# Kernel tuning notes

Measured on AMD Instinct MI355X. Metric: run time of the kernel, lower is better.

Reference implementation:

```python
import jax, jax.numpy as jnp
import numpy as np

LOGIT_SCALE = 1.0
REDUCTION = "mean"

N, H, V = 4096, 512, 50257


def setup_inputs() -> dict:
    key = jax.random.key(0)
    k1, k2, k3, k4 = jax.random.split(key, 4)
    x = jax.random.normal(k1, (N, H), dtype=jnp.float32)
    targets = jax.random.normal(k2, (N, V), dtype=jnp.float32)
    weight = jax.random.normal(k3, (V, H), dtype=jnp.float32) * 0.02
    bias = jax.random.normal(k4, (V,), dtype=jnp.float32) * 0.02
    return {"x": x, "targets": targets, "weight": weight, "bias": bias}


def reference(x, targets, weight, bias):
    # logits = x @ W^T + b  -> [N, V]
    logits = jnp.einsum("nh,vh->nv", x, weight) + bias
    scaled = logits * LOGIT_SCALE
    # logsumexp over vocab for both predicted and target logits (fp32)
    lse_logits = jax.nn.logsumexp(scaled, axis=-1)                      # [N]
    lse_targets = jax.nn.logsumexp(targets, axis=-1)                    # [N]
    # original: .nan_to_num(nan=inf) -> rows with nan targets contribute 0
    lse_targets = jnp.where(jnp.isnan(lse_targets), jnp.inf, lse_targets)
    p_target = jnp.exp(targets - lse_targets[:, None])                  # softmax(targets)
    log_p_pred = scaled - lse_logits[:, None]                           # log_softmax(scaled logits)
    per_row_loss = -jnp.sum(p_target * log_p_pred, axis=-1)             # [N]
    loss = per_row_loss.sum()
    if REDUCTION == "mean":
        loss = loss / N
    return loss
```

## Files before the change

kernel.cpp:

```cpp
#include <hip/hip_runtime.h>
#include <hip/hip_bf16.h>

#define N_ROWS 4096
#define H_DIM  512
#define V_DIM  50257
#define BM 128
#define BN 128
#define BK 64
#define NSTEP (H_DIM / BK)
#define VT_TOTAL 393
#define V_PAD (VT_TOTAL * BN)
#define NCHUNK 131
#define LOG2E 1.4426950408889634f
#define BUF0 0
#define BUF1 32768
#define LBASE 32768

#define VMCNT8() asm volatile("s_waitcnt vmcnt(8)" ::: "memory")
#define VMCNT0() asm volatile("s_waitcnt vmcnt(0)" ::: "memory")
#define LGKM0()  asm volatile("s_waitcnt lgkmcnt(0)" ::: "memory")
#define BARRIER() __builtin_amdgcn_s_barrier()

typedef __attribute__((ext_vector_type(8))) short short8;
typedef __attribute__((ext_vector_type(4))) float f32x4;

static __device__ __forceinline__ unsigned short f2bf(float f) {
  unsigned u = __float_as_uint(f);
  u = (u + 0x7fffu + ((u >> 16) & 1u)) >> 16;
  return (unsigned short)u;
}

static __device__ __forceinline__ void gload_lds16(const void* g, void* l) {
  __builtin_amdgcn_global_load_lds(
      (const __attribute__((address_space(1))) void*)g,
      (__attribute__((address_space(3))) void*)l, 16, 0, 0);
}

__global__ void convert_kernel(const float* __restrict__ X,
                               const float* __restrict__ W,
                               __hip_bfloat16* __restrict__ Xb,
                               __hip_bfloat16* __restrict__ Wb) {
  const long wtot8 = (long)V_PAD * H_DIM / 8;
  const long xtot8 = (long)N_ROWS * H_DIM / 8;
  long i = (long)blockIdx.x * blockDim.x + threadIdx.x;
  unsigned short o[8];
  if (i < wtot8) {
    long base = i * 8;
    long row = base >> 9;
    if (row < V_DIM) {
      const float4* s = (const float4*)(W + base);
      float4 a = s[0], b = s[1];
      o[0]=f2bf(a.x); o[1]=f2bf(a.y); o[2]=f2bf(a.z); o[3]=f2bf(a.w);
      o[4]=f2bf(b.x); o[5]=f2bf(b.y); o[6]=f2bf(b.z); o[7]=f2bf(b.w);
    } else {
      #pragma unroll
      for (int k = 0; k < 8; ++k) o[k] = 0;
    }
    *(short8*)(Wb + base) = *(const short8*)o;
  } else if (i < wtot8 + xtot8) {
    long base = (i - wtot8) * 8;
    const float4* s = (const float4*)(X + base);
    float4 a = s[0], b = s[1];
    o[0]=f2bf(a.x); o[1]=f2bf(a.y); o[2]=f2bf(a.z); o[3]=f2bf(a.w);
    o[4]=f2bf(b.x); o[5]=f2bf(b.y); o[6]=f2bf(b.z); o[7]=f2bf(b.w);
    *(short8*)(Xb + base) = *(const short8*)o;
  }
}

template <bool GUARD>
static __device__ __forceinline__ void chunk_stats(
    const float (&Lraw)[16], const f32x4 (&T)[4], int gcol0,
    float& mlr, float& slr, float& mtr, float& str, float& ddr) {
  float Lv[16], Tv[16];
  #pragma unroll
  for (int k = 0; k < 16; ++k) {
    const bool ok = !GUARD || (gcol0 + k < V_DIM);
    Lv[k] = ok ? Lraw[k] : -1e30f;
    Tv[k] = ok ? T[k >> 2][k & 3] : -1e30f;
  }
  float g = Lv[0];
  #pragma unroll
  for (int k = 1; k < 16; ++k) g = fmaxf(g, Lv[k]);
  if (g > mlr + 12.f) { slr *= exp2f((mlr - g) * LOG2E); mlr = g; }
  float bl = mlr * LOG2E;
  float ss = 0.f;
  #pragma unroll
  for (int k = 0; k < 16; ++k) ss += exp2f(__builtin_fmaf(Lv[k], LOG2E, -bl));
  slr += ss;
  float gt = Tv[0];
  #pragma unroll
  for (int k = 1; k < 16; ++k) gt = fmaxf(gt, Tv[k]);
  if (gt > mtr + 12.f) {
    float sc = exp2f((mtr - gt) * LOG2E);
    str *= sc; ddr *= sc; mtr = gt;
  }
  float bt = mtr * LOG2E;
  float s2 = 0.f, d2 = 0.f;
  #pragma unroll
  for (int k = 0; k < 16; ++k) {
    float e = exp2f(__builtin_fmaf(Tv[k], LOG2E, -bt));
    s2 += e;
    d2 = __builtin_fmaf(e, Lv[k], d2);
  }
  str += s2; ddr += d2;
}

template <bool GUARD>
static __device__ __forceinline__ void stream_tile(
    const float* __restrict__ targets, const char* __restrict__ Lrow,
    long growVD, int vbase, int cb0, int rsw, long tlim,
    float& mlr, float& slr, float& mtr, float& str, float& ddr) {
  f32x4 T0[4], T1[4];
  auto LOADT = [&](f32x4 (&D)[4], int i) {
    #pragma unroll
    for (int c = 0; c < 4; ++c) {
      long off = growVD + vbase + cb0 + i * 16 + c * 4;
      if (GUARD) off = off > tlim ? tlim : off;
      D[c] = *(const f32x4*)(targets + off);
    }
  };
  auto DOCHUNK = [&](const f32x4 (&T)[4], int i) {
    const int ob = (cb0 << 1) + (i << 5);
    short8 l0 = *(const short8*)(Lrow + ((ob) ^ rsw));
    short8 l1 = *(const short8*)(Lrow + ((ob + 16) ^ rsw));
    float Lraw[16];
    #pragma unroll
    for (int e = 0; e < 8; ++e) {
      Lraw[e]     = __uint_as_float(((unsigned)(unsigned short)l0[e]) << 16);
      Lraw[e + 8] = __uint_as_float(((unsigned)(unsigned short)l1[e]) << 16);
    }
    chunk_stats<GUARD>(Lraw, T, vbase + cb0 + i * 16, mlr, slr, mtr, str, ddr);
  };
  LOADT(T0, 0); LOADT(T1, 1);
  DOCHUNK(T0, 0);
  LOADT(T0, 2);
  DOCHUNK(T1, 1);
  LOADT(T1, 3);
  DOCHUNK(T0, 2);
  DOCHUNK(T1, 3);
}

__global__ __launch_bounds__(256, 2)
void fused_kernel(const __hip_bfloat16* __restrict__ Xb,
                  const __hip_bfloat16* __restrict__ Wb,
                  const float* __restrict__ bias,
                  const float* __restrict__ targets,
                  float* __restrict__ partials) {
  __shared__ __align__(16) char smem[65536];

  const int tid  = threadIdx.x;
  const int lane = tid & 63;
  const int wid  = tid >> 6;
  const int wm   = wid >> 1;
  const int wn   = wid & 1;
  const int q    = lane >> 4;
  const int c15  = lane & 15;
  const int brow = blockIdx.x;
  const int chunk = blockIdx.y;

  float mlr = -1e30f, slr = 0.f, mtr = -1e30f, str = 0.f, ddr = 0.f;

  const int srow8 = tid >> 3;
  const int soff  = ((tid & 7) * 8) ^ ((srow8 & 7) * 8);
  const __hip_bfloat16* asrc = Xb + (long)(brow * BM + srow8) * H_DIM + soff;

  const int rm      = (c15 & 7) << 4;
  const int arow_b  = (wm * 64 + c15) * 128;
  const int brow_b  = (wn * 64 + c15) * 128;

  auto stage = [&](int bufb, const __hip_bfloat16* a_s,
                   const __hip_bfloat16* b_s, int kk) {
    #pragma unroll
    for (int i = 0; i < 4; ++i)
      gload_lds16(a_s + (long)i * 32 * H_DIM + kk,
                  smem + bufb + i * 4096 + tid * 16);
    #pragma unroll
    for (int i = 0; i < 4; ++i)
      gload_lds16(b_s + (long)i * 32 * H_DIM + kk,
                  smem + bufb + 16384 + i * 4096 + tid * 16);
  };

  const int srow  = tid >> 1;
  const int shalf = tid & 1;
  const int cb0   = shalf * 64;
  const long grow   = (long)(brow * BM + srow);
  const long growVD = grow * V_DIM;
  const long tlim   = (long)N_ROWS * V_DIM - 4;
  const char* Lrow  = smem + LBASE + srow * 256;
  const int rsw     = (srow & 7) << 4;

  const __hip_bfloat16* bsrc = Wb + (long)(chunk * BN + srow8) * H_DIM + soff;
  stage(BUF0, asrc, bsrc, 0);

  #pragma unroll 1
  for (int vt = chunk; vt < VT_TOTAL; vt += NCHUNK) {
    const int vbase = vt * BN;
    const int v0 = vbase + wn * 64 + q * 4;
    const bool last = (vt + NCHUNK >= VT_TOTAL);
    const __hip_bfloat16* bsrc_next =
        Wb + (long)((vt + NCHUNK) * BN + srow8) * H_DIM + soff;

    f32x4 acc[4][4];
    #pragma unroll
    for (int a = 0; a < 4; ++a)
      #pragma unroll
      for (int b = 0; b < 4; ++b)
        acc[a][b] = (f32x4){0.f, 0.f, 0.f, 0.f};

    #pragma unroll
    for (int ks = 0; ks < NSTEP; ++ks) {
      const int cb = (ks & 1) ? BUF1 : BUF0;
      const int nb = cb ^ 32768;
      if (ks < NSTEP - 1)
        stage(nb, asrc, bsrc, (ks + 1) * BK);
      else if (!last)
        stage(nb, asrc, bsrc_next, 0);

      if (ks == NSTEP - 1 && last) { VMCNT0(); } else { VMCNT8(); }
      BARRIER();

      #pragma unroll
      for (int s = 0; s < 2; ++s) {
        short8 xf[4], wf[4];
        #pragma unroll
        for (int a = 0; a < 4; ++a)
          xf[a] = *(const short8*)(smem + cb + arow_b + a * 2048 +
                                   ((s * 64 + q * 16) ^ rm));
        #pragma unroll
        for (int b = 0; b < 4; ++b)
          wf[b] = *(const short8*)(smem + cb + 16384 + brow_b + b * 2048 +
                                   ((s * 64 + q * 16) ^ rm));
        __builtin_amdgcn_s_setprio(1);
        #pragma unroll
        for (int a = 0; a < 4; ++a)
          #pragma unroll
          for (int b = 0; b < 4; ++b)
            acc[a][b] = __builtin_amdgcn_mfma_f32_16x16x32_bf16(
                wf[b], xf[a], acc[a][b], 0, 0, 0);
        __builtin_amdgcn_s_setprio(0);
      }
      LGKM0();
      BARRIER();
    }
    bsrc = bsrc_next;

    f32x4 bp[4];
    #pragma unroll
    for (int b = 0; b < 4; ++b) {
      int bo = v0 + b * 16;
      bo = bo > (V_DIM - 4) ? (V_DIM - 4) : bo;
      bp[b] = *(const f32x4*)(bias + bo);
    }
    #pragma unroll
    for (int a = 0; a < 4; ++a) {
      const int row = wm * 64 + a * 16 + c15;
      char* rb = smem + LBASE + row * 256;
      #pragma unroll
      for (int b = 0; b < 4; ++b) {
        uint2 w;
        w.x = (unsigned)f2bf(acc[a][b][0] + bp[b][0]) |
              ((unsigned)f2bf(acc[a][b][1] + bp[b][1]) << 16);
        w.y = (unsigned)f2bf(acc[a][b][2] + bp[b][2]) |
              ((unsigned)f2bf(acc[a][b][3] + bp[b][3]) << 16);
        const int o = wn * 128 + b * 32 + q * 8;
        *(uint2*)(rb + (o ^ rm)) = w;
      }
    }
    LGKM0();
    BARRIER();

    if (vt == VT_TOTAL - 1)
      stream_tile<true >(targets, Lrow, growVD, vbase, cb0, rsw, tlim,
                         mlr, slr, mtr, str, ddr);
    else
      stream_tile<false>(targets, Lrow, growVD, vbase, cb0, rsw, tlim,
                         mlr, slr, mtr, str, ddr);
    LGKM0();
    BARRIER();
  }

  {
    float ml2 = __shfl_xor(mlr, 1);
    float sl2 = __shfl_xor(slr, 1);
    float mt2 = __shfl_xor(mtr, 1);
    float st2 = __shfl_xor(str, 1);
    float dd2 = __shfl_xor(ddr, 1);
    float nm = fmaxf(mlr, ml2);
    float slo = slr * exp2f((mlr - nm) * LOG2E) + sl2 * exp2f((ml2 - nm) * LOG2E);
    float nmt = fmaxf(mtr, mt2);
    float e1 = exp2f((mtr - nmt) * LOG2E);
    float e2 = exp2f((mt2 - nmt) * LOG2E);
    float sto = str * e1 + st2 * e2;
    float ddo = ddr * e1 + dd2 * e2;
    if (shalf == 0) {
      float* o = partials + (grow * NCHUNK + chunk) * 5;
      o[0] = nm; o[1] = slo; o[2] = nmt; o[3] = sto; o[4] = ddo;
    }
  }
}

__global__ void rowloss_kernel(const float* __restrict__ partials,
                               float* __restrict__ rowloss) {
  int r = blockIdx.x * blockDim.x + threadIdx.x;
  if (r >= N_ROWS) return;
  const float* p = partials + (long)r * NCHUNK * 5;
  float ml = -1e30f, sl = 0.f, mt = -1e30f, st = 0.f, dd = 0.f;
  for (int c = 0; c < NCHUNK; ++c) {
    float ml2 = p[0], sl2 = p[1], mt2 = p[2], st2 = p[3], dd2 = p[4];
    p += 5;
    float nm = fmaxf(ml, ml2);
    sl = sl * exp2f((ml - nm) * LOG2E) + sl2 * exp2f((ml2 - nm) * LOG2E);
    ml = nm;
    float nmt = fmaxf(mt, mt2);
    float e1 = exp2f((mt - nmt) * LOG2E);
    float e2 = exp2f((mt2 - nmt) * LOG2E);
    st = st * e1 + st2 * e2;
    dd = dd * e1 + dd2 * e2;
    mt = nmt;
  }
  float lse = ml + logf(sl);
  rowloss[r] = lse - dd / st;
}

__global__ void final_kernel(const float* __restrict__ rowloss,
                             float* __restrict__ out) {
  __shared__ float sm[4];
  float s = 0.f;
  for (int i = threadIdx.x; i < N_ROWS; i += 256) s += rowloss[i];
  #pragma unroll
  for (int off = 32; off > 0; off >>= 1) s += __shfl_down(s, off);
  if ((threadIdx.x & 63) == 0) sm[threadIdx.x >> 6] = s;
  __syncthreads();
  if (threadIdx.x == 0) out[0] = (sm[0] + sm[1] + sm[2] + sm[3]) * (1.0f / (float)N_ROWS);
}

extern "C" void kernel_launch(void* const* d_in, const int* in_sizes, int n_in,
                              void* d_out, int out_size, void* d_ws, size_t ws_size,
                              hipStream_t stream) {
  const float* x       = (const float*)d_in[0];
  const float* targets = (const float*)d_in[1];
  const float* weight  = (const float*)d_in[2];
  const float* bias    = (const float*)d_in[3];
  float* out = (float*)d_out;

  char* ws = (char*)d_ws;
  __hip_bfloat16* Wb = (__hip_bfloat16*)ws;
  size_t off = (size_t)V_PAD * H_DIM * 2;
  __hip_bfloat16* Xb = (__hip_bfloat16*)(ws + off);
  off += (size_t)N_ROWS * H_DIM * 2;
  float* partials = (float*)(ws + off);
  off += (size_t)N_ROWS * NCHUNK * 5 * sizeof(float);
  float* rowloss = (float*)(ws + off);

  convert_kernel<<<13600, 256, 0, stream>>>(x, weight, Xb, Wb);
  dim3 grid(N_ROWS / BM, NCHUNK);
  fused_kernel<<<grid, 256, 0, stream>>>(Xb, Wb, bias, targets, partials);
  rowloss_kernel<<<N_ROWS / 256, 256, 0, stream>>>(partials, rowloss);
  final_kernel<<<1, 256, 0, stream>>>(rowloss, out);
}
```

Baseline: 558.1 us.

## Double fused kernel block to 512 threads with 2x4 wave grid

Raises the fused GEMM+softmax kernel from 256 to 512 threads per block, splitting the 128x128 tile over 8 waves (each 64x32) and letting four threads share each row when streaming targets. Staging loads, the vmcnt wait count, the LDS layout offsets and the final shuffle reduction are adjusted to match, and the setprio hints are dropped. The aim is more waves in flight to hide latency on the bandwidth-bound targets stream. In exchange each wave does fewer MFMAs per LDS fragment read, so there is more LDS traffic per FLOP and more barrier cost per block.

```diff
diff --git a/kernel.cpp b/kernel.cpp
--- a/kernel.cpp
+++ b/kernel.cpp
@@ -16,7 +16,7 @@
 #define BUF1 32768
 #define LBASE 32768
 
-#define VMCNT8() asm volatile("s_waitcnt vmcnt(8)" ::: "memory")
+#define VMCNT4() asm volatile("s_waitcnt vmcnt(4)" ::: "memory")
 #define VMCNT0() asm volatile("s_waitcnt vmcnt(0)" ::: "memory")
 #define LGKM0()  asm volatile("s_waitcnt lgkmcnt(0)" ::: "memory")
 #define BARRIER() __builtin_amdgcn_s_barrier()
@@ -108,19 +108,24 @@
 template <bool GUARD>
 static __device__ __forceinline__ void stream_tile(
     const float* __restrict__ targets, const char* __restrict__ Lrow,
-    long growVD, int vbase, int cb0, int rsw, long tlim,
+    long growVD, int vbase, int q32, int rsw, long tlim,
     float& mlr, float& slr, float& mtr, float& str, float& ddr) {
   f32x4 T0[4], T1[4];
-  auto LOADT = [&](f32x4 (&D)[4], int i) {
-    #pragma unroll
-    for (int c = 0; c < 4; ++c) {
-      long off = growVD + vbase + cb0 + i * 16 + c * 4;
-      if (GUARD) off = off > tlim ? tlim : off;
-      D[c] = *(const f32x4*)(targets + off);
-    }
-  };
-  auto DOCHUNK = [&](const f32x4 (&T)[4], int i) {
-    const int ob = (cb0 << 1) + (i << 5);
+  #pragma unroll
+  for (int c = 0; c < 4; ++c) {
+    long off = growVD + vbase + q32 + c * 4;
+    if (GUARD) off = off > tlim ? tlim : off;
+    T0[c] = *(const f32x4*)(targets + off);
+  }
+  #pragma unroll
+  for (int c = 0; c < 4; ++c) {
+    long off = growVD + vbase + q32 + 16 + c * 4;
+    if (GUARD) off = off > tlim ? tlim : off;
+    T1[c] = *(const f32x4*)(targets + off);
+  }
+  #pragma unroll
+  for (int i = 0; i < 2; ++i) {
+    const int ob = (q32 << 1) + (i << 5);
     short8 l0 = *(const short8*)(Lrow + ((ob) ^ rsw));
     short8 l1 = *(const short8*)(Lrow + ((ob + 16) ^ rsw));
     float Lraw[16];
@@ -129,18 +134,14 @@
       Lraw[e]     = __uint_as_float(((unsigned)(unsigned short)l0[e]) << 16);
       Lraw[e + 8] = __uint_as_float(((unsigned)(unsigned short)l1[e]) << 16);
     }
-    chunk_stats<GUARD>(Lraw, T, vbase + cb0 + i * 16, mlr, slr, mtr, str, ddr);
-  };
-  LOADT(T0, 0); LOADT(T1, 1);
-  DOCHUNK(T0, 0);
-  LOADT(T0, 2);
-  DOCHUNK(T1, 1);
-  LOADT(T1, 3);
-  DOCHUNK(T0, 2);
-  DOCHUNK(T1, 3);
-}
-
-__global__ __launch_bounds__(256, 2)
+    if (i == 0)
+      chunk_stats<GUARD>(Lraw, T0, vbase + q32,      mlr, slr, mtr, str, ddr);
+    else
+      chunk_stats<GUARD>(Lraw, T1, vbase + q32 + 16, mlr, slr, mtr, str, ddr);
+  }
+}
+
+__global__ __launch_bounds__(512, 4)
 void fused_kernel(const __hip_bfloat16* __restrict__ Xb,
                   const __hip_bfloat16* __restrict__ Wb,
                   const float* __restrict__ bias,
@@ -151,8 +152,8 @@
   const int tid  = threadIdx.x;
   const int lane = tid & 63;
   const int wid  = tid >> 6;
-  const int wm   = wid >> 1;
-  const int wn   = wid & 1;
+  const int wm   = wid >> 2;
+  const int wn   = wid & 3;
   const int q    = lane >> 4;
   const int c15  = lane & 15;
   const int brow = blockIdx.x;
@@ -161,28 +162,28 @@
   float mlr = -1e30f, slr = 0.f, mtr = -1e30f, str = 0.f, ddr = 0.f;
 
   const int srow8 = tid >> 3;
-  const int soff  = ((tid & 7) * 8) ^ ((srow8 & 7) * 8);
+  const int soff  = ((tid & 7) ^ (srow8 & 7)) * 8;
   const __hip_bfloat16* asrc = Xb + (long)(brow * BM + srow8) * H_DIM + soff;
 
   const int rm      = (c15 & 7) << 4;
   const int arow_b  = (wm * 64 + c15) * 128;
-  const int brow_b  = (wn * 64 + c15) * 128;
+  const int brow_b  = (wn * 32 + c15) * 128;
 
   auto stage = [&](int bufb, const __hip_bfloat16* a_s,
                    const __hip_bfloat16* b_s, int kk) {
     #pragma unroll
-    for (int i = 0; i < 4; ++i)
-      gload_lds16(a_s + (long)i * 32 * H_DIM + kk,
-                  smem + bufb + i * 4096 + tid * 16);
-    #pragma unroll
-    for (int i = 0; i < 4; ++i)
-      gload_lds16(b_s + (long)i * 32 * H_DIM + kk,
-                  smem + bufb + 16384 + i * 4096 + tid * 16);
+    for (int i = 0; i < 2; ++i)
+      gload_lds16(a_s + (long)i * 64 * H_DIM + kk,
+                  smem + bufb + i * 8192 + tid * 16);
+    #pragma unroll
+    for (int i = 0; i < 2; ++i)
+      gload_lds16(b_s + (long)i * 64 * H_DIM + kk,
+                  smem + bufb + 16384 + i * 8192 + tid * 16);
   };
 
-  const int srow  = tid >> 1;
-  const int shalf = tid & 1;
-  const int cb0   = shalf * 64;
+  const int srow  = tid >> 2;
+  const int quart = tid & 3;
+  const int q32   = quart * 32;
   const long grow   = (long)(brow * BM + srow);
   const long growVD = grow * V_DIM;
   const long tlim   = (long)N_ROWS * V_DIM - 4;
@@ -195,16 +196,16 @@
   #pragma unroll 1
   for (int vt = chunk; vt < VT_TOTAL; vt += NCHUNK) {
     const int vbase = vt * BN;
-    const int v0 = vbase + wn * 64 + q * 4;
+    const int v0 = vbase + wn * 32 + q * 4;
     const bool last = (vt + NCHUNK >= VT_TOTAL);
     const __hip_bfloat16* bsrc_next =
         Wb + (long)((vt + NCHUNK) * BN + srow8) * H_DIM + soff;
 
-    f32x4 acc[4][4];
+    f32x4 acc[4][2];
     #pragma unroll
     for (int a = 0; a < 4; ++a)
       #pragma unroll
-      for (int b = 0; b < 4; ++b)
+      for (int b = 0; b < 2; ++b)
         acc[a][b] = (f32x4){0.f, 0.f, 0.f, 0.f};
 
     #pragma unroll
@@ -216,37 +217,35 @@
       else if (!last)
         stage(nb, asrc, bsrc_next, 0);
 
-      if (ks == NSTEP - 1 && last) { VMCNT0(); } else { VMCNT8(); }
+      if (ks == NSTEP - 1 && last) { VMCNT0(); } else { VMCNT4(); }
       BARRIER();
 
       #pragma unroll
       for (int s = 0; s < 2; ++s) {
-        short8 xf[4], wf[4];
+        short8 xf[4], wf[2];
         #pragma unroll
         for (int a = 0; a < 4; ++a)
           xf[a] = *(const short8*)(smem + cb + arow_b + a * 2048 +
                                    ((s * 64 + q * 16) ^ rm));
         #pragma unroll
-        for (int b = 0; b < 4; ++b)
+        for (int b = 0; b < 2; ++b)
           wf[b] = *(const short8*)(smem + cb + 16384 + brow_b + b * 2048 +
                                    ((s * 64 + q * 16) ^ rm));
-        __builtin_amdgcn_s_setprio(1);
         #pragma unroll
         for (int a = 0; a < 4; ++a)
           #pragma unroll
-          for (int b = 0; b < 4; ++b)
+          for (int b = 0; b < 2; ++b)
             acc[a][b] = __builtin_amdgcn_mfma_f32_16x16x32_bf16(
                 wf[b], xf[a], acc[a][b], 0, 0, 0);
-        __builtin_amdgcn_s_setprio(0);
       }
       LGKM0();
       BARRIER();
     }
     bsrc = bsrc_next;
 
-    f32x4 bp[4];
-    #pragma unroll
-    for (int b = 0; b < 4; ++b) {
+    f32x4 bp[2];
+    #pragma unroll
+    for (int b = 0; b < 2; ++b) {
       int bo = v0 + b * 16;
       bo = bo > (V_DIM - 4) ? (V_DIM - 4) : bo;
       bp[b] = *(const f32x4*)(bias + bo);
@@ -256,13 +255,13 @@
       const int row = wm * 64 + a * 16 + c15;
       char* rb = smem + LBASE + row * 256;
       #pragma unroll
-      for (int b = 0; b < 4; ++b) {
+      for (int b = 0; b < 2; ++b) {
         uint2 w;
         w.x = (unsigned)f2bf(acc[a][b][0] + bp[b][0]) |
               ((unsigned)f2bf(acc[a][b][1] + bp[b][1]) << 16);
         w.y = (unsigned)f2bf(acc[a][b][2] + bp[b][2]) |
               ((unsigned)f2bf(acc[a][b][3] + bp[b][3]) << 16);
-        const int o = wn * 128 + b * 32 + q * 8;
+        const int o = wn * 64 + b * 32 + q * 8;
         *(uint2*)(rb + (o ^ rm)) = w;
       }
     }
@@ -270,32 +269,35 @@
     BARRIER();
 
     if (vt == VT_TOTAL - 1)
-      stream_tile<true >(targets, Lrow, growVD, vbase, cb0, rsw, tlim,
+      stream_tile<true >(targets, Lrow, growVD, vbase, q32, rsw, tlim,
                          mlr, slr, mtr, str, ddr);
     else
-      stream_tile<false>(targets, Lrow, growVD, vbase, cb0, rsw, tlim,
+      stream_tile<false>(targets, Lrow, growVD, vbase, q32, rsw, tlim,
                          mlr, slr, mtr, str, ddr);
     LGKM0();
     BARRIER();
   }
 
-  {
-    float ml2 = __shfl_xor(mlr, 1);
-    float sl2 = __shfl_xor(slr, 1);
-    float mt2 = __shfl_xor(mtr, 1);
-    float st2 = __shfl_xor(str, 1);
-    float dd2 = __shfl_xor(ddr, 1);
+  #pragma unroll
+  for (int off = 1; off <= 2; off <<= 1) {
+    float ml2 = __shfl_xor(mlr, off);
+    float sl2 = __shfl_xor(slr, off);
+    float mt2 = __shfl_xor(mtr, off);
+    float st2 = __shfl_xor(str, off);
+    float dd2 = __shfl_xor(ddr, off);
     float nm = fmaxf(mlr, ml2);
-    float slo = slr * exp2f((mlr - nm) * LOG2E) + sl2 * exp2f((ml2 - nm) * LOG2E);
+    slr = slr * exp2f((mlr - nm) * LOG2E) + sl2 * exp2f((ml2 - nm) * LOG2E);
+    mlr = nm;
     float nmt = fmaxf(mtr, mt2);
     float e1 = exp2f((mtr - nmt) * LOG2E);
     float e2 = exp2f((mt2 - nmt) * LOG2E);
-    float sto = str * e1 + st2 * e2;
-    float ddo = ddr * e1 + dd2 * e2;
-    if (shalf == 0) {
-      float* o = partials + (grow * NCHUNK + chunk) * 5;
-      o[0] = nm; o[1] = slo; o[2] = nmt; o[3] = sto; o[4] = ddo;
-    }
+    str = str * e1 + st2 * e2;
+    ddr = ddr * e1 + dd2 * e2;
+    mtr = nmt;
+  }
+  if (quart == 0) {
+    float* o = partials + (grow * NCHUNK + chunk) * 5;
+    o[0] = mlr; o[1] = slr; o[2] = mtr; o[3] = str; o[4] = ddr;
   }
 }
 
@@ -354,7 +356,7 @@
 
   convert_kernel<<<13600, 256, 0, stream>>>(x, weight, Xb, Wb);
   dim3 grid(N_ROWS / BM, NCHUNK);
-  fused_kernel<<<grid, 256, 0, stream>>>(Xb, Wb, bias, targets, partials);
+  fused_kernel<<<grid, 512, 0, stream>>>(Xb, Wb, bias, targets, partials);
   rowloss_kernel<<<N_ROWS / 256, 256, 0, stream>>>(partials, rowloss);
   final_kernel<<<1, 256, 0, stream>>>(rowloss, out);
 }
```

New measurement: 537.3 us. -3.7%, faster.

## Deepen GEMM pipeline to four stages and split logits streaming into halves

Applied to the files above, without the earlier changes.

Halves the K-step to 32 and uses a four-buffer LDS ring with three stages prefetched ahead, waiting on graded vmcnt values. Logits are now written to shared memory one 64-row half at a time, so the targets load for the second half overlaps the stats pass over the first. The smaller LDS logits region frees space for the deeper ring. Each thread now covers a quarter of a row, and partials are merged with a two-level shuffle. This is meant to hide global-load latency in both the GEMM and the targets stream, at the cost of more barriers and more waits per tile.

```diff
diff --git a/kernel.cpp b/kernel.cpp
--- a/kernel.cpp
+++ b/kernel.cpp
@@ -6,23 +6,28 @@
 #define V_DIM  50257
 #define BM 128
 #define BN 128
-#define BK 64
-#define NSTEP (H_DIM / BK)
+#define BK 32
+#define NSTEP 16
 #define VT_TOTAL 393
 #define V_PAD (VT_TOTAL * BN)
 #define NCHUNK 131
 #define LOG2E 1.4426950408889634f
-#define BUF0 0
-#define BUF1 32768
-#define LBASE 32768
-
-#define VMCNT8() asm volatile("s_waitcnt vmcnt(8)" ::: "memory")
-#define VMCNT0() asm volatile("s_waitcnt vmcnt(0)" ::: "memory")
+#define LOFF 49152
+
 #define LGKM0()  asm volatile("s_waitcnt lgkmcnt(0)" ::: "memory")
+#define VMC0()   asm volatile("s_waitcnt vmcnt(0)" ::: "memory")
 #define BARRIER() __builtin_amdgcn_s_barrier()
 
 typedef __attribute__((ext_vector_type(8))) short short8;
 typedef __attribute__((ext_vector_type(4))) float f32x4;
+
+template <int N>
+static __device__ __forceinline__ void vmw() {
+  if constexpr (N == 0)       asm volatile("s_waitcnt vmcnt(0)" ::: "memory");
+  else if constexpr (N == 4)  asm volatile("s_waitcnt vmcnt(4)" ::: "memory");
+  else if constexpr (N == 8)  asm volatile("s_waitcnt vmcnt(8)" ::: "memory");
+  else                        asm volatile("s_waitcnt vmcnt(12)" ::: "memory");
+}
 
 static __device__ __forceinline__ unsigned short f2bf(float f) {
   unsigned u = __float_as_uint(f);
@@ -68,33 +73,33 @@
 }
 
 template <bool GUARD>
-static __device__ __forceinline__ void chunk_stats(
-    const float (&Lraw)[16], const f32x4 (&T)[4], int gcol0,
-    float& mlr, float& slr, float& mtr, float& str, float& ddr) {
+static __device__ __forceinline__ void stats16(
+    const float (&Lraw)[16], const f32x4* T4, int gcol0,
+    float& ml, float& sl, float& mt, float& st, float& dd) {
   float Lv[16], Tv[16];
   #pragma unroll
   for (int k = 0; k < 16; ++k) {
     const bool ok = !GUARD || (gcol0 + k < V_DIM);
     Lv[k] = ok ? Lraw[k] : -1e30f;
-    Tv[k] = ok ? T[k >> 2][k & 3] : -1e30f;
+    Tv[k] = ok ? T4[k >> 2][k & 3] : -1e30f;
   }
   float g = Lv[0];
   #pragma unroll
   for (int k = 1; k < 16; ++k) g = fmaxf(g, Lv[k]);
-  if (g > mlr + 12.f) { slr *= exp2f((mlr - g) * LOG2E); mlr = g; }
-  float bl = mlr * LOG2E;
+  if (g > ml + 12.f) { sl *= exp2f((ml - g) * LOG2E); ml = g; }
+  float bl = ml * LOG2E;
   float ss = 0.f;
   #pragma unroll
   for (int k = 0; k < 16; ++k) ss += exp2f(__builtin_fmaf(Lv[k], LOG2E, -bl));
-  slr += ss;
+  sl += ss;
   float gt = Tv[0];
   #pragma unroll
   for (int k = 1; k < 16; ++k) gt = fmaxf(gt, Tv[k]);
-  if (gt > mtr + 12.f) {
-    float sc = exp2f((mtr - gt) * LOG2E);
-    str *= sc; ddr *= sc; mtr = gt;
-  }
-  float bt = mtr * LOG2E;
+  if (gt > mt + 12.f) {
+    float sc = exp2f((mt - gt) * LOG2E);
+    st *= sc; dd *= sc; mt = gt;
+  }
+  float bt = mt * LOG2E;
   float s2 = 0.f, d2 = 0.f;
   #pragma unroll
   for (int k = 0; k < 16; ++k) {
@@ -102,26 +107,17 @@
     s2 += e;
     d2 = __builtin_fmaf(e, Lv[k], d2);
   }
-  str += s2; ddr += d2;
+  st += s2; dd += d2;
 }
 
 template <bool GUARD>
-static __device__ __forceinline__ void stream_tile(
-    const float* __restrict__ targets, const char* __restrict__ Lrow,
-    long growVD, int vbase, int cb0, int rsw, long tlim,
-    float& mlr, float& slr, float& mtr, float& str, float& ddr) {
-  f32x4 T0[4], T1[4];
-  auto LOADT = [&](f32x4 (&D)[4], int i) {
-    #pragma unroll
-    for (int c = 0; c < 4; ++c) {
-      long off = growVD + vbase + cb0 + i * 16 + c * 4;
-      if (GUARD) off = off > tlim ? tlim : off;
-      D[c] = *(const f32x4*)(targets + off);
-    }
-  };
-  auto DOCHUNK = [&](const f32x4 (&T)[4], int i) {
-    const int ob = (cb0 << 1) + (i << 5);
-    short8 l0 = *(const short8*)(Lrow + ((ob) ^ rsw));
+static __device__ __forceinline__ void stream_pass(
+    const f32x4 (&t)[8], const char* Lrow, int rsw, int obbase, int gc0,
+    float& ml, float& sl, float& mt, float& st, float& dd) {
+  #pragma unroll
+  for (int ch = 0; ch < 2; ++ch) {
+    const int ob = obbase + ch * 32;
+    short8 l0 = *(const short8*)(Lrow + (ob ^ rsw));
     short8 l1 = *(const short8*)(Lrow + ((ob + 16) ^ rsw));
     float Lraw[16];
     #pragma unroll
@@ -129,15 +125,8 @@
       Lraw[e]     = __uint_as_float(((unsigned)(unsigned short)l0[e]) << 16);
       Lraw[e + 8] = __uint_as_float(((unsigned)(unsigned short)l1[e]) << 16);
     }
-    chunk_stats<GUARD>(Lraw, T, vbase + cb0 + i * 16, mlr, slr, mtr, str, ddr);
-  };
-  LOADT(T0, 0); LOADT(T1, 1);
-  DOCHUNK(T0, 0);
-  LOADT(T0, 2);
-  DOCHUNK(T1, 1);
-  LOADT(T1, 3);
-  DOCHUNK(T0, 2);
-  DOCHUNK(T1, 3);
+    stats16<GUARD>(Lraw, &t[ch * 4], gc0 + ch * 16, ml, sl, mt, st, dd);
+  }
 }
 
 __global__ __launch_bounds__(256, 2)
@@ -158,47 +147,46 @@
   const int brow = blockIdx.x;
   const int chunk = blockIdx.y;
 
-  float mlr = -1e30f, slr = 0.f, mtr = -1e30f, str = 0.f, ddr = 0.f;
-
-  const int srow8 = tid >> 3;
-  const int soff  = ((tid & 7) * 8) ^ ((srow8 & 7) * 8);
-  const __hip_bfloat16* asrc = Xb + (long)(brow * BM + srow8) * H_DIM + soff;
-
-  const int rm      = (c15 & 7) << 4;
-  const int arow_b  = (wm * 64 + c15) * 128;
-  const int brow_b  = (wn * 64 + c15) * 128;
-
-  auto stage = [&](int bufb, const __hip_bfloat16* a_s,
-                   const __hip_bfloat16* b_s, int kk) {
-    #pragma unroll
-    for (int i = 0; i < 4; ++i)
-      gload_lds16(a_s + (long)i * 32 * H_DIM + kk,
-                  smem + bufb + i * 4096 + tid * 16);
-    #pragma unroll
-    for (int i = 0; i < 4; ++i)
-      gload_lds16(b_s + (long)i * 32 * H_DIM + kk,
-                  smem + bufb + 16384 + i * 4096 + tid * 16);
+  float ml0 = -1e30f, sl0 = 0.f, mt0 = -1e30f, st0 = 0.f, dd0 = 0.f;
+  float ml1 = -1e30f, sl1 = 0.f, mt1 = -1e30f, st1 = 0.f, dd1 = 0.f;
+
+  const int srow = tid >> 2;
+  const int sq   = (tid & 3) ^ (srow & 3);
+  const __hip_bfloat16* xsrc =
+      Xb + (long)(brow * BM + srow) * H_DIM + sq * 8;
+  const long woff = (long)srow * H_DIM + sq * 8;
+
+  const int xbyte = (wm * 64 + c15) * 64 + ((q ^ (c15 & 3)) * 16);
+  const int wbyte = (wn * 64 + c15) * 64 + ((q ^ (c15 & 3)) * 16);
+
+  const int quart = tid & 3;
+  const int q32   = quart * 32;
+  const int obb   = q32 * 2;
+  const int rsw   = (srow & 15) << 4;
+  const char* Lrow = smem + LOFF + srow * 256;
+  const long tlim  = (long)N_ROWS * V_DIM - 4;
+
+  auto stage = [&](int bufb, const __hip_bfloat16* wsrcp, int kk) {
+    gload_lds16(xsrc + kk,                smem + bufb + tid * 16);
+    gload_lds16(xsrc + 64 * H_DIM + kk,   smem + bufb + 4096 + tid * 16);
+    gload_lds16(wsrcp + woff + kk,        smem + bufb + 8192 + tid * 16);
+    gload_lds16(wsrcp + woff + 64 * H_DIM + kk,
+                smem + bufb + 12288 + tid * 16);
   };
 
-  const int srow  = tid >> 1;
-  const int shalf = tid & 1;
-  const int cb0   = shalf * 64;
-  const long grow   = (long)(brow * BM + srow);
-  const long growVD = grow * V_DIM;
-  const long tlim   = (long)N_ROWS * V_DIM - 4;
-  const char* Lrow  = smem + LBASE + srow * 256;
-  const int rsw     = (srow & 7) << 4;
-
-  const __hip_bfloat16* bsrc = Wb + (long)(chunk * BN + srow8) * H_DIM + soff;
-  stage(BUF0, asrc, bsrc, 0);
+  const __hip_bfloat16* wsrc = Wb + (long)chunk * BN * H_DIM;
+  stage(0, wsrc, 0);
+  stage(16384, wsrc, BK);
+  stage(32768, wsrc, 2 * BK);
 
   #pragma unroll 1
-  for (int vt = chunk; vt < VT_TOTAL; vt += NCHUNK) {
+  for (int ti = 0; ti < 3; ++ti) {
+    const int vt = chunk + ti * NCHUNK;
     const int vbase = vt * BN;
     const int v0 = vbase + wn * 64 + q * 4;
-    const bool last = (vt + NCHUNK >= VT_TOTAL);
-    const __hip_bfloat16* bsrc_next =
-        Wb + (long)((vt + NCHUNK) * BN + srow8) * H_DIM + soff;
+    const bool last = (ti == 2);
+    const bool guard = (vt == VT_TOTAL - 1);
+    const __hip_bfloat16* wsrc_next = Wb + (long)(vt + NCHUNK) * BN * H_DIM;
 
     f32x4 acc[4][4];
     #pragma unroll
@@ -209,40 +197,38 @@
 
     #pragma unroll
     for (int ks = 0; ks < NSTEP; ++ks) {
-      const int cb = (ks & 1) ? BUF1 : BUF0;
-      const int nb = cb ^ 32768;
-      if (ks < NSTEP - 1)
-        stage(nb, asrc, bsrc, (ks + 1) * BK);
+      const int bb = (ks & 3) << 14;
+      const int pb = ((ks + 3) & 3) << 14;
+      if (ks < 13)
+        stage(pb, wsrc, (ks + 3) * BK);
       else if (!last)
-        stage(nb, asrc, bsrc_next, 0);
-
-      if (ks == NSTEP - 1 && last) { VMCNT0(); } else { VMCNT8(); }
+        stage(pb, wsrc_next, (ks - 13) * BK);
+
+      if (ks < 13)       vmw<12>();
+      else if (!last)    vmw<12>();
+      else if (ks == 13) vmw<8>();
+      else if (ks == 14) vmw<4>();
+      else               vmw<0>();
       BARRIER();
 
-      #pragma unroll
-      for (int s = 0; s < 2; ++s) {
-        short8 xf[4], wf[4];
-        #pragma unroll
-        for (int a = 0; a < 4; ++a)
-          xf[a] = *(const short8*)(smem + cb + arow_b + a * 2048 +
-                                   ((s * 64 + q * 16) ^ rm));
+      short8 xf[4], wf[4];
+      #pragma unroll
+      for (int a = 0; a < 4; ++a)
+        xf[a] = *(const short8*)(smem + bb + xbyte + a * 1024);
+      #pragma unroll
+      for (int b = 0; b < 4; ++b)
+        wf[b] = *(const short8*)(smem + bb + 8192 + wbyte + b * 1024);
+      #pragma unroll
+      for (int a = 0; a < 4; ++a)
         #pragma unroll
         for (int b = 0; b < 4; ++b)
-          wf[b] = *(const short8*)(smem + cb + 16384 + brow_b + b * 2048 +
-                                   ((s * 64 + q * 16) ^ rm));
-        __builtin_amdgcn_s_setprio(1);
-        #pragma unroll
-        for (int a = 0; a < 4; ++a)
-          #pragma unroll
-          for (int b = 0; b < 4; ++b)
-            acc[a][b] = __builtin_amdgcn_mfma_f32_16x16x32_bf16(
-                wf[b], xf[a], acc[a][b], 0, 0, 0);
-        __builtin_amdgcn_s_setprio(0);
-      }
+          acc[a][b] = __builtin_amdgcn_mfma_f32_16x16x32_bf16(
+              wf[b], xf[a], acc[a][b], 0, 0, 0);
+
       LGKM0();
       BARRIER();
     }
-    bsrc = bsrc_next;
+    wsrc = wsrc_next;
 
     f32x4 bp[4];
     #pragma unroll
@@ -251,51 +237,96 @@
       bo = bo > (V_DIM - 4) ? (V_DIM - 4) : bo;
       bp[b] = *(const f32x4*)(bias + bo);
     }
-    #pragma unroll
-    for (int a = 0; a < 4; ++a) {
-      const int row = wm * 64 + a * 16 + c15;
-      char* rb = smem + LBASE + row * 256;
-      #pragma unroll
-      for (int b = 0; b < 4; ++b) {
-        uint2 w;
-        w.x = (unsigned)f2bf(acc[a][b][0] + bp[b][0]) |
-              ((unsigned)f2bf(acc[a][b][1] + bp[b][1]) << 16);
-        w.y = (unsigned)f2bf(acc[a][b][2] + bp[b][2]) |
-              ((unsigned)f2bf(acc[a][b][3] + bp[b][3]) << 16);
-        const int o = wn * 128 + b * 32 + q * 8;
-        *(uint2*)(rb + (o ^ rm)) = w;
+    auto loadT = [&](f32x4 (&t)[8], int h) {
+      const long rb =
+          (long)(brow * BM + h * 64 + srow) * V_DIM + vbase + q32;
+      #pragma unroll
+      for (int c = 0; c < 8; ++c) {
+        long off = rb + c * 4;
+        off = off > tlim ? tlim : off;
+        t[c] = *(const f32x4*)(targets + off);
       }
-    }
+    };
+    auto dump_half = [&]() {
+      #pragma unroll
+      for (int a = 0; a < 4; ++a) {
+        const int r = a * 16 + c15;
+        char* rb = smem + LOFF + r * 256;
+        const int rw = (r & 15) << 4;
+        #pragma unroll
+        for (int b = 0; b < 4; ++b) {
+          uint2 w;
+          w.x = (unsigned)f2bf(acc[a][b][0] + bp[b][0]) |
+                ((unsigned)f2bf(acc[a][b][1] + bp[b][1]) << 16);
+          w.y = (unsigned)f2bf(acc[a][b][2] + bp[b][2]) |
+                ((unsigned)f2bf(acc[a][b][3] + bp[b][3]) << 16);
+          const int o = wn * 128 + b * 32 + q * 8;
+          *(uint2*)(rb + (o ^ rw)) = w;
+        }
+      }
+    };
+
+    f32x4 t0[8];
+    loadT(t0, 0);
+    if (wm == 0) dump_half();
     LGKM0();
     BARRIER();
-
-    if (vt == VT_TOTAL - 1)
-      stream_tile<true >(targets, Lrow, growVD, vbase, cb0, rsw, tlim,
-                         mlr, slr, mtr, str, ddr);
+    VMC0();
+    f32x4 t1[8];
+    loadT(t1, 1);
+    if (guard)
+      stream_pass<true >(t0, Lrow, rsw, obb, vbase + q32, ml0, sl0, mt0, st0, dd0);
     else
-      stream_tile<false>(targets, Lrow, growVD, vbase, cb0, rsw, tlim,
-                         mlr, slr, mtr, str, ddr);
+      stream_pass<false>(t0, Lrow, rsw, obb, vbase + q32, ml0, sl0, mt0, st0, dd0);
     LGKM0();
     BARRIER();
-  }
-
-  {
-    float ml2 = __shfl_xor(mlr, 1);
-    float sl2 = __shfl_xor(slr, 1);
-    float mt2 = __shfl_xor(mtr, 1);
-    float st2 = __shfl_xor(str, 1);
-    float dd2 = __shfl_xor(ddr, 1);
-    float nm = fmaxf(mlr, ml2);
-    float slo = slr * exp2f((mlr - nm) * LOG2E) + sl2 * exp2f((ml2 - nm) * LOG2E);
-    float nmt = fmaxf(mtr, mt2);
-    float e1 = exp2f((mtr - nmt) * LOG2E);
-    float e2 = exp2f((mt2 - nmt) * LOG2E);
-    float sto = str * e1 + st2 * e2;
-    float ddo = ddr * e1 + dd2 * e2;
-    if (shalf == 0) {
-      float* o = partials + (grow * NCHUNK + chunk) * 5;
-      o[0] = nm; o[1] = slo; o[2] = nmt; o[3] = sto; o[4] = ddo;
-    }
+    if (wm == 1) dump_half();
+    LGKM0();
+    BARRIER();
+    VMC0();
+    if (guard)
+      stream_pass<true >(t1, Lrow, rsw, obb, vbase + q32, ml1, sl1, mt1, st1, dd1);
+    else
+      stream_pass<false>(t1, Lrow, rsw, obb, vbase + q32, ml1, sl1, mt1, st1, dd1);
+    LGKM0();
+    BARRIER();
+  }
+
+  #pragma unroll
+  for (int off = 1; off <= 2; off <<= 1) {
+    {
+      float ml2 = __shfl_xor(ml0, off), sl2 = __shfl_xor(sl0, off);
+      float mt2 = __shfl_xor(mt0, off), st2 = __shfl_xor(st0, off);
+      float dd2 = __shfl_xor(dd0, off);
+      float nm = fmaxf(ml0, ml2);
+      sl0 = sl0 * exp2f((ml0 - nm) * LOG2E) + sl2 * exp2f((ml2 - nm) * LOG2E);
+      ml0 = nm;
+      float nmt = fmaxf(mt0, mt2);
+      float e1 = exp2f((mt0 - nmt) * LOG2E), e2 = exp2f((mt2 - nmt) * LOG2E);
+      st0 = st0 * e1 + st2 * e2;
+      dd0 = dd0 * e1 + dd2 * e2;
+      mt0 = nmt;
+    }
+    {
+      float ml2 = __shfl_xor(ml1, off), sl2 = __shfl_xor(sl1, off);
+      float mt2 = __shfl_xor(mt1, off), st2 = __shfl_xor(st1, off);
+      float dd2 = __shfl_xor(dd1, off);
+      float nm = fmaxf(ml1, ml2);
+      sl1 = sl1 * exp2f((ml1 - nm) * LOG2E) + sl2 * exp2f((ml2 - nm) * LOG2E);
+      ml1 = nm;
+      float nmt = fmaxf(mt1, mt2);
+      float e1 = exp2f((mt1 - nmt) * LOG2E), e2 = exp2f((mt2 - nmt) * LOG2E);
+      st1 = st1 * e1 + st2 * e2;
+      dd1 = dd1 * e1 + dd2 * e2;
+      mt1 = nmt;
+    }
+  }
+  if (quart == 0) {
+    long r0 = (long)(brow * BM + srow);
+    float* o = partials + (r0 * NCHUNK + chunk) * 5;
+    o[0] = ml0; o[1] = sl0; o[2] = mt0; o[3] = st0; o[4] = dd0;
+    float* o1 = partials + ((r0 + 64) * NCHUNK + chunk) * 5;
+    o1[0] = ml1; o1[1] = sl1; o1[2] = mt1; o1[3] = st1; o1[4] = dd1;
   }
 }
 
```

Measured after the change: 778.0 us. 39.4% more time.

## Enlarge fused GEMM tile to 256x256 with one vocab tile per block

Applied to the files above, without the earlier changes.

The fused GEMM and softmax kernel moves from 128x128 tiles, where each block looped over three vocab tiles and prefetched across them, to 256x256 tiles with 512 threads and 128 KB of dynamic LDS. Each block now handles a single vocab chunk. The larger tile raises MFMA work per loaded byte and halves how many times X and W are read. In exchange it drops the cross-tile prefetch overlap and the setprio hints, needs two passes to stage logits through LDS, and doubles the size of the partials array. With 128 KB LDS per block, the 2-blocks-per-CU launch bound may not be reachable, so occupancy could drop.

```diff
diff --git a/kernel.cpp b/kernel.cpp
--- a/kernel.cpp
+++ b/kernel.cpp
@@ -4,25 +4,27 @@
 #define N_ROWS 4096
 #define H_DIM  512
 #define V_DIM  50257
-#define BM 128
-#define BN 128
+#define BM 256
+#define BN 256
 #define BK 64
-#define NSTEP (H_DIM / BK)
-#define VT_TOTAL 393
-#define V_PAD (VT_TOTAL * BN)
-#define NCHUNK 131
+#define NSTEP 8
+#define VCH 197
+#define V_PAD (VCH * 256)
 #define LOG2E 1.4426950408889634f
-#define BUF0 0
-#define BUF1 32768
-#define LBASE 32768
-
-#define VMCNT8() asm volatile("s_waitcnt vmcnt(8)" ::: "memory")
-#define VMCNT0() asm volatile("s_waitcnt vmcnt(0)" ::: "memory")
+#define BUFSZ 65536
+#define SMEM_BYTES 131072
+
 #define LGKM0()  asm volatile("s_waitcnt lgkmcnt(0)" ::: "memory")
 #define BARRIER() __builtin_amdgcn_s_barrier()
 
 typedef __attribute__((ext_vector_type(8))) short short8;
 typedef __attribute__((ext_vector_type(4))) float f32x4;
+
+template <int N>
+static __device__ __forceinline__ void vmw() {
+  if constexpr (N == 0)      asm volatile("s_waitcnt vmcnt(0)" ::: "memory");
+  else                       asm volatile("s_waitcnt vmcnt(8)" ::: "memory");
+}
 
 static __device__ __forceinline__ unsigned short f2bf(float f) {
   unsigned u = __float_as_uint(f);
@@ -68,33 +70,33 @@
 }
 
 template <bool GUARD>
-static __device__ __forceinline__ void chunk_stats(
-    const float (&Lraw)[16], const f32x4 (&T)[4], int gcol0,
-    float& mlr, float& slr, float& mtr, float& str, float& ddr) {
+static __device__ __forceinline__ void stats16(
+    const float (&Lraw)[16], const f32x4* T4, int gcol0,
+    float& ml, float& sl, float& mt, float& st, float& dd) {
   float Lv[16], Tv[16];
   #pragma unroll
   for (int k = 0; k < 16; ++k) {
     const bool ok = !GUARD || (gcol0 + k < V_DIM);
     Lv[k] = ok ? Lraw[k] : -1e30f;
-    Tv[k] = ok ? T[k >> 2][k & 3] : -1e30f;
+    Tv[k] = ok ? T4[k >> 2][k & 3] : -1e30f;
   }
   float g = Lv[0];
   #pragma unroll
   for (int k = 1; k < 16; ++k) g = fmaxf(g, Lv[k]);
-  if (g > mlr + 12.f) { slr *= exp2f((mlr - g) * LOG2E); mlr = g; }
-  float bl = mlr * LOG2E;
+  if (g > ml + 12.f) { sl *= exp2f((ml - g) * LOG2E); ml = g; }
+  float bl = ml * LOG2E;
   float ss = 0.f;
   #pragma unroll
   for (int k = 0; k < 16; ++k) ss += exp2f(__builtin_fmaf(Lv[k], LOG2E, -bl));
-  slr += ss;
+  sl += ss;
   float gt = Tv[0];
   #pragma unroll
   for (int k = 1; k < 16; ++k) gt = fmaxf(gt, Tv[k]);
-  if (gt > mtr + 12.f) {
-    float sc = exp2f((mtr - gt) * LOG2E);
-    str *= sc; ddr *= sc; mtr = gt;
-  }
-  float bt = mtr * LOG2E;
+  if (gt > mt + 12.f) {
+    float sc = exp2f((mt - gt) * LOG2E);
+    st *= sc; dd *= sc; mt = gt;
+  }
+  float bt = mt * LOG2E;
   float s2 = 0.f, d2 = 0.f;
   #pragma unroll
   for (int k = 0; k < 16; ++k) {
@@ -102,26 +104,26 @@
     s2 += e;
     d2 = __builtin_fmaf(e, Lv[k], d2);
   }
-  str += s2; ddr += d2;
+  st += s2; dd += d2;
 }
 
 template <bool GUARD>
-static __device__ __forceinline__ void stream_tile(
+static __device__ __forceinline__ void stream_seg(
     const float* __restrict__ targets, const char* __restrict__ Lrow,
-    long growVD, int vbase, int cb0, int rsw, long tlim,
-    float& mlr, float& slr, float& mtr, float& str, float& ddr) {
+    long tbase, int gcol0, int lbyte0, int rsw, long tlim,
+    float& ml, float& sl, float& mt, float& st, float& dd) {
   f32x4 T0[4], T1[4];
   auto LOADT = [&](f32x4 (&D)[4], int i) {
     #pragma unroll
     for (int c = 0; c < 4; ++c) {
-      long off = growVD + vbase + cb0 + i * 16 + c * 4;
+      long off = tbase + i * 16 + c * 4;
       if (GUARD) off = off > tlim ? tlim : off;
       D[c] = *(const f32x4*)(targets + off);
     }
   };
   auto DOCHUNK = [&](const f32x4 (&T)[4], int i) {
-    const int ob = (cb0 << 1) + (i << 5);
-    short8 l0 = *(const short8*)(Lrow + ((ob) ^ rsw));
+    const int ob = lbyte0 + (i << 5);
+    short8 l0 = *(const short8*)(Lrow + (ob ^ rsw));
     short8 l1 = *(const short8*)(Lrow + ((ob + 16) ^ rsw));
     float Lraw[16];
     #pragma unroll
@@ -129,7 +131,7 @@
       Lraw[e]     = __uint_as_float(((unsigned)(unsigned short)l0[e]) << 16);
       Lraw[e + 8] = __uint_as_float(((unsigned)(unsigned short)l1[e]) << 16);
     }
-    chunk_stats<GUARD>(Lraw, T, vbase + cb0 + i * 16, mlr, slr, mtr, str, ddr);
+    stats16<GUARD>(Lraw, T, gcol0 + i * 16, ml, sl, mt, st, dd);
   };
   LOADT(T0, 0); LOADT(T1, 1);
   DOCHUNK(T0, 0);
@@ -140,160 +142,151 @@
   DOCHUNK(T1, 3);
 }
 
-__global__ __launch_bounds__(256, 2)
+__global__ __launch_bounds__(512, 2)
 void fused_kernel(const __hip_bfloat16* __restrict__ Xb,
                   const __hip_bfloat16* __restrict__ Wb,
                   const float* __restrict__ bias,
                   const float* __restrict__ targets,
                   float* __restrict__ partials) {
-  __shared__ __align__(16) char smem[65536];
+  extern __shared__ __align__(16) char smem[];
 
   const int tid  = threadIdx.x;
   const int lane = tid & 63;
   const int wid  = tid >> 6;
-  const int wm   = wid >> 1;
-  const int wn   = wid & 1;
+  const int wm   = wid >> 2;
+  const int wn   = wid & 3;
   const int q    = lane >> 4;
   const int c15  = lane & 15;
   const int brow = blockIdx.x;
-  const int chunk = blockIdx.y;
-
-  float mlr = -1e30f, slr = 0.f, mtr = -1e30f, str = 0.f, ddr = 0.f;
+  const int vchunk = blockIdx.y;
+  const int vbase = vchunk * BN;
+
+  float ml = -1e30f, sl = 0.f, mt = -1e30f, st = 0.f, dd = 0.f;
 
   const int srow8 = tid >> 3;
-  const int soff  = ((tid & 7) * 8) ^ ((srow8 & 7) * 8);
+  const int soff  = ((tid & 7) ^ (srow8 & 7)) * 8;
   const __hip_bfloat16* asrc = Xb + (long)(brow * BM + srow8) * H_DIM + soff;
-
-  const int rm      = (c15 & 7) << 4;
-  const int arow_b  = (wm * 64 + c15) * 128;
-  const int brow_b  = (wn * 64 + c15) * 128;
-
-  auto stage = [&](int bufb, const __hip_bfloat16* a_s,
-                   const __hip_bfloat16* b_s, int kk) {
+  const __hip_bfloat16* wsrc = Wb + (long)(vbase + srow8) * H_DIM + soff;
+
+  const int rm     = (c15 & 7) << 4;
+  const int arow_b = (wm * 128 + c15) * 128;
+  const int brow_b = (wn * 64 + c15) * 128;
+
+  auto stage = [&](int bufb, int kk) {
     #pragma unroll
     for (int i = 0; i < 4; ++i)
-      gload_lds16(a_s + (long)i * 32 * H_DIM + kk,
-                  smem + bufb + i * 4096 + tid * 16);
+      gload_lds16(asrc + (long)i * 64 * H_DIM + kk,
+                  smem + bufb + i * 8192 + tid * 16);
     #pragma unroll
     for (int i = 0; i < 4; ++i)
-      gload_lds16(b_s + (long)i * 32 * H_DIM + kk,
-                  smem + bufb + 16384 + i * 4096 + tid * 16);
+      gload_lds16(wsrc + (long)i * 64 * H_DIM + kk,
+                  smem + bufb + 32768 + i * 8192 + tid * 16);
   };
 
-  const int srow  = tid >> 1;
-  const int shalf = tid & 1;
-  const int cb0   = shalf * 64;
-  const long grow   = (long)(brow * BM + srow);
-  const long growVD = grow * V_DIM;
-  const long tlim   = (long)N_ROWS * V_DIM - 4;
-  const char* Lrow  = smem + LBASE + srow * 256;
-  const int rsw     = (srow & 7) << 4;
-
-  const __hip_bfloat16* bsrc = Wb + (long)(chunk * BN + srow8) * H_DIM + soff;
-  stage(BUF0, asrc, bsrc, 0);
-
-  #pragma unroll 1
-  for (int vt = chunk; vt < VT_TOTAL; vt += NCHUNK) {
-    const int vbase = vt * BN;
-    const int v0 = vbase + wn * 64 + q * 4;
-    const bool last = (vt + NCHUNK >= VT_TOTAL);
-    const __hip_bfloat16* bsrc_next =
-        Wb + (long)((vt + NCHUNK) * BN + srow8) * H_DIM + soff;
-
-    f32x4 acc[4][4];
-    #pragma unroll
-    for (int a = 0; a < 4; ++a)
+  stage(0, 0);
+
+  f32x4 acc[8][4];
+  #pragma unroll
+  for (int a = 0; a < 8; ++a)
+    #pragma unroll
+    for (int b = 0; b < 4; ++b)
+      acc[a][b] = (f32x4){0.f, 0.f, 0.f, 0.f};
+
+  #pragma unroll
+  for (int ks = 0; ks < NSTEP; ++ks) {
+    const int cb = (ks & 1) ? BUFSZ : 0;
+    if (ks < NSTEP - 1) stage(cb ^ BUFSZ, (ks + 1) * BK);
+
+    if (ks == NSTEP - 1) vmw<0>(); else vmw<8>();
+    BARRIER();
+
+    #pragma unroll
+    for (int s = 0; s < 2; ++s) {
+      short8 xf[8], wf[4];
+      #pragma unroll
+      for (int a = 0; a < 8; ++a)
+        xf[a] = *(const short8*)(smem + cb + arow_b + a * 2048 +
+                                 ((s * 64 + q * 16) ^ rm));
       #pragma unroll
       for (int b = 0; b < 4; ++b)
-        acc[a][b] = (f32x4){0.f, 0.f, 0.f, 0.f};
-
-    #pragma unroll
-    for (int ks = 0; ks < NSTEP; ++ks) {
-      const int cb = (ks & 1) ? BUF1 : BUF0;
-      const int nb = cb ^ 32768;
-      if (ks < NSTEP - 1)
-        stage(nb, asrc, bsrc, (ks + 1) * BK);
-      else if (!last)
-        stage(nb, asrc, bsrc_next, 0);
-
-      if (ks == NSTEP - 1 && last) { VMCNT0(); } else { VMCNT8(); }
-      BARRIER();
-
-      #pragma unroll
-      for (int s = 0; s < 2; ++s) {
-        short8 xf[4], wf[4];
-        #pragma unroll
-        for (int a = 0; a < 4; ++a)
-          xf[a] = *(const short8*)(smem + cb + arow_b + a * 2048 +
-                                   ((s * 64 + q * 16) ^ rm));
+        wf[b] = *(const short8*)(smem + cb + 32768 + brow_b + b * 2048 +
+                                 ((s * 64 + q * 16) ^ rm));
+      #pragma unroll
+      for (int a = 0; a < 8; ++a)
         #pragma unroll
         for (int b = 0; b < 4; ++b)
-          wf[b] = *(const short8*)(smem + cb + 16384 + brow_b + b * 2048 +
-                                   ((s * 64 + q * 16) ^ rm));
-        __builtin_amdgcn_s_setprio(1);
-        #pragma unroll
-        for (int a = 0; a < 4; ++a)
-          #pragma unroll
-          for (int b = 0; b < 4; ++b)
-            acc[a][b] = __builtin_amdgcn_mfma_f32_16x16x32_bf16(
-                wf[b], xf[a], acc[a][b], 0, 0, 0);
-        __builtin_amdgcn_s_setprio(0);
-      }
-      LGKM0();
-      BARRIER();
-    }
-    bsrc = bsrc_next;
-
-    f32x4 bp[4];
+          acc[a][b] = __builtin_amdgcn_mfma_f32_16x16x32_bf16(
+              wf[b], xf[a], acc[a][b], 0, 0, 0);
+    }
+    LGKM0();
+    BARRIER();
+  }
+
+  f32x4 bp[4];
+  {
+    const int v0 = vbase + wn * 64 + q * 4;
     #pragma unroll
     for (int b = 0; b < 4; ++b) {
       int bo = v0 + b * 16;
       bo = bo > (V_DIM - 4) ? (V_DIM - 4) : bo;
       bp[b] = *(const f32x4*)(bias + bo);
     }
-    #pragma unroll
-    for (int a = 0; a < 4; ++a) {
-      const int row = wm * 64 + a * 16 + c15;
-      char* rb = smem + LBASE + row * 256;
-      #pragma unroll
-      for (int b = 0; b < 4; ++b) {
-        uint2 w;
-        w.x = (unsigned)f2bf(acc[a][b][0] + bp[b][0]) |
-              ((unsigned)f2bf(acc[a][b][1] + bp[b][1]) << 16);
-        w.y = (unsigned)f2bf(acc[a][b][2] + bp[b][2]) |
-              ((unsigned)f2bf(acc[a][b][3] + bp[b][3]) << 16);
-        const int o = wn * 128 + b * 32 + q * 8;
-        *(uint2*)(rb + (o ^ rm)) = w;
+  }
+
+  const int srow  = tid >> 1;
+  const int seg   = tid & 1;
+  const long grow = (long)(brow * BM + srow);
+  const long tlim = (long)N_ROWS * V_DIM - 4;
+  const char* Lrow = smem + srow * 256;
+  const int rsw    = (srow & 7) << 4;
+  const int lbyte0 = seg * 128;
+  const bool guard = (vbase + BN > V_DIM);
+
+  #pragma unroll
+  for (int h = 0; h < 2; ++h) {
+    if ((wn >> 1) == h) {
+      #pragma unroll
+      for (int a = 0; a < 8; ++a) {
+        const int row = wm * 128 + a * 16 + c15;
+        char* rb = smem + row * 256;
+        #pragma unroll
+        for (int b = 0; b < 4; ++b) {
+          uint2 w;
+          w.x = (unsigned)f2bf(acc[a][b][0] + bp[b][0]) |
+                ((unsigned)f2bf(acc[a][b][1] + bp[b][1]) << 16);
+          w.y = (unsigned)f2bf(acc[a][b][2] + bp[b][2]) |
+                ((unsigned)f2bf(acc[a][b][3] + bp[b][3]) << 16);
+          const int o = (wn & 1) * 128 + b * 32 + q * 8;
+          *(uint2*)(rb + (o ^ rm)) = w;
+        }
       }
     }
     LGKM0();
     BARRIER();
 
-    if (vt == VT_TOTAL - 1)
-      stream_tile<true >(targets, Lrow, growVD, vbase, cb0, rsw, tlim,
-                         mlr, slr, mtr, str, ddr);
+    const int gcol0 = vbase + h * 128 + seg * 64;
+    const long tbase = grow * V_DIM + gcol0;
+    if (guard)
+      stream_seg<true >(targets, Lrow, tbase, gcol0, lbyte0, rsw, tlim,
+                        ml, sl, mt, st, dd);
     else
-      stream_tile<false>(targets, Lrow, growVD, vbase, cb0, rsw, tlim,
-                         mlr, slr, mtr, str, ddr);
-    LGKM0();
+      stream_seg<false>(targets, Lrow, tbase, gcol0, lbyte0, rsw, tlim,
+                        ml, sl, mt, st, dd);
     BARRIER();
   }
 
   {
-    float ml2 = __shfl_xor(mlr, 1);
-    float sl2 = __shfl_xor(slr, 1);
-    float mt2 = __shfl_xor(mtr, 1);
-    float st2 = __shfl_xor(str, 1);
-    float dd2 = __shfl_xor(ddr, 1);
-    float nm = fmaxf(mlr, ml2);
-    float slo = slr * exp2f((mlr - nm) * LOG2E) + sl2 * exp2f((ml2 - nm) * LOG2E);
-    float nmt = fmaxf(mtr, mt2);
-    float e1 = exp2f((mtr - nmt) * LOG2E);
-    float e2 = exp2f((mt2 - nmt) * LOG2E);
-    float sto = str * e1 + st2 * e2;
-    float ddo = ddr * e1 + dd2 * e2;
-    if (shalf == 0) {
-      float* o = partials + (grow * NCHUNK + chunk) * 5;
+    float ml2 = __shfl_xor(ml, 1), sl2 = __shfl_xor(sl, 1);
+    float mt2 = __shfl_xor(mt, 1), st2 = __shfl_xor(st, 1);
+    float dd2 = __shfl_xor(dd, 1);
+    float nm = fmaxf(ml, ml2);
+    float slo = sl * exp2f((ml - nm) * LOG2E) + sl2 * exp2f((ml2 - nm) * LOG2E);
+    float nmt = fmaxf(mt, mt2);
+    float e1 = exp2f((mt - nmt) * LOG2E), e2 = exp2f((mt2 - nmt) * LOG2E);
+    float sto = st * e1 + st2 * e2;
+    float ddo = dd * e1 + dd2 * e2;
+    if (seg == 0) {
+      float* o = partials + (grow * VCH + vchunk) * 5;
       o[0] = nm; o[1] = slo; o[2] = nmt; o[3] = sto; o[4] = ddo;
     }
   }
@@ -303,9 +296,9 @@
                                float* __restrict__ rowloss) {
   int r = blockIdx.x * blockDim.x + threadIdx.x;
   if (r >= N_ROWS) return;
-  const float* p = partials + (long)r * NCHUNK * 5;
+  const float* p = partials + (long)r * VCH * 5;
   float ml = -1e30f, sl = 0.f, mt = -1e30f, st = 0.f, dd = 0.f;
-  for (int c = 0; c < NCHUNK; ++c) {
+  for (int c = 0; c < VCH; ++c) {
     float ml2 = p[0], sl2 = p[1], mt2 = p[2], st2 = p[3], dd2 = p[4];
     p += 5;
     float nm = fmaxf(ml, ml2);
@@ -349,12 +342,16 @@
   __hip_bfloat16* Xb = (__hip_bfloat16*)(ws + off);
   off += (size_t)N_ROWS * H_DIM * 2;
   float* partials = (float*)(ws + off);
-  off += (size_t)N_ROWS * NCHUNK * 5 * sizeof(float);
+  off += (size_t)N_ROWS * VCH * 5 * sizeof(float);
   float* rowloss = (float*)(ws + off);
 
-  convert_kernel<<<13600, 256, 0, stream>>>(x, weight, Xb, Wb);
-  dim3 grid(N_ROWS / BM, NCHUNK);
-  fused_kernel<<<grid, 256, 0, stream>>>(Xb, Wb, bias, targets, partials);
+  (void)hipFuncSetAttribute((const void*)fused_kernel,
+                            hipFuncAttributeMaxDynamicSharedMemorySize,
+                            SMEM_BYTES);
+
+  convert_kernel<<<13632, 256, 0, stream>>>(x, weight, Xb, Wb);
+  dim3 grid(N_ROWS / BM, VCH);
+  fused_kernel<<<grid, 512, SMEM_BYTES, stream>>>(Xb, Wb, bias, targets, partials);
   rowloss_kernel<<<N_ROWS / 256, 256, 0, stream>>>(partials, rowloss);
   final_kernel<<<1, 256, 0, stream>>>(rowloss, out);
 }
```

Measured after the change: 605.3 us. 1.08x slower.
